# Performance work log

Hardware: AMD Instinct MI355X
Metric: run time of the kernel (lower is better)

## Reference

```python
import jax, jax.numpy as jnp
import numpy as np

EMBED_DIM = 1024
NUM_HEADS = 16
HEAD_DIM = EMBED_DIM // NUM_HEADS  # used only for the softmax scale


def setup_inputs() -> dict:
    key = jax.random.key(0)
    k_x, k_wqkv, k_bqkv, k_wo, k_bo = jax.random.split(key, 5)
    bound_qkv = 1.0 / np.sqrt(EMBED_DIM)
    return {
        "x": jax.random.normal(k_x, (4, 2048, EMBED_DIM), dtype=jnp.float32),
        "W_qkv": jax.random.uniform(k_wqkv, (EMBED_DIM, 3 * EMBED_DIM), jnp.float32, -bound_qkv, bound_qkv),
        "b_qkv": jax.random.uniform(k_bqkv, (3 * EMBED_DIM,), jnp.float32, -bound_qkv, bound_qkv),
        "W_out": jax.random.uniform(k_wo, (EMBED_DIM, EMBED_DIM), jnp.float32, -bound_qkv, bound_qkv),
        "b_out": jax.random.uniform(k_bo, (EMBED_DIM,), jnp.float32, -bound_qkv, bound_qkv),
    }


def reference(x, W_qkv, b_qkv, W_out, b_out):
    # fused QKV projection: [B,S,3E]
    qkv = jnp.einsum("bse,ef->bsf", x, W_qkv) + b_qkv
    q, k, v = jnp.split(qkv, 3, axis=-1)  # each [B,S,E]
    scale = 1.0 / jnp.sqrt(jnp.float32(HEAD_DIM))
    # NOTE: no head reshape — attention over full embed_dim, scale uses head_dim
    scores = jnp.einsum("bqe,bke->bqk", q, k) * scale  # [B,S,S]
    attn = jax.nn.softmax(scores, axis=-1)
    context = jnp.einsum("bqk,bke->bqe", attn, v)  # [B,S,E]
    return jnp.einsum("bse,ef->bsf", context, W_out) + b_out
```

## Files before the change

kernel.cpp:

```cpp
#include <hip/hip_runtime.h>

typedef unsigned short u16;
typedef __bf16   bf16x8 __attribute__((ext_vector_type(8)));
typedef float    f32x4  __attribute__((ext_vector_type(4)));
typedef unsigned short u16x4 __attribute__((ext_vector_type(4)));

__device__ inline float bf2f(u16 u) { return __uint_as_float(((unsigned int)u) << 16); }
__device__ inline u16 f2bf(float f) {
    unsigned int u = __float_as_uint(f);
    u += 0x7FFF + ((u >> 16) & 1);
    return (u16)(u >> 16);
}

__device__ inline void gl2lds16(const u16* g, u16* l) {
    __builtin_amdgcn_global_load_lds(
        (const __attribute__((address_space(1))) void*)g,
        (__attribute__((address_space(3))) void*)l, 16, 0, 0);
}

__global__ void sniff_dtype(const u16* __restrict__ x, int* __restrict__ flag) {
    const int lane = threadIdx.x;
    const unsigned idx = lane * 131072u + 65536u;
    const u16 u = x[idx];
    const int e = (u >> 7) & 0xFF;
    const unsigned long long b = __ballot(e >= 100 && e <= 140);
    if (lane == 0) flag[0] = (__popcll(b) >= 48) ? 0 : 1;
}

__global__ __launch_bounds__(256)
void convx(const void* __restrict__ in, u16* __restrict__ out, const int* __restrict__ flagp) {
    const long i = ((long)blockIdx.x * 256 + threadIdx.x) * 4;
    if (*flagp) {
        f32x4 v = *(const f32x4*)((const float*)in + i);
        u16x4 o; o[0] = f2bf(v[0]); o[1] = f2bf(v[1]); o[2] = f2bf(v[2]); o[3] = f2bf(v[3]);
        *(u16x4*)(out + i) = o;
    } else {
        *(u16x4*)(out + i) = *(const u16x4*)((const u16*)in + i);
    }
}

__global__ __launch_bounds__(256)
void conv_biases(const void* __restrict__ b1, const void* __restrict__ b2,
                 u16* __restrict__ o1, u16* __restrict__ o2,
                 const int* __restrict__ flagp) {
    const int i = blockIdx.x * 256 + threadIdx.x;
    const int f = *flagp;
    if (i < 3072) o1[i] = f ? f2bf(((const float*)b1)[i]) : ((const u16*)b1)[i];
    else { const int j = i - 3072;
           o2[j] = f ? f2bf(((const float*)b2)[j]) : ((const u16*)b2)[j]; }
}

template <int GM, int GN, int WM, int WN, int OUT_MODE, bool HAS_BIAS>
__global__ __launch_bounds__(256, 4)
void gemm_t(const u16* __restrict__ A, const u16* __restrict__ Bt,
            void* __restrict__ Cv, const u16* __restrict__ bias,
            int K, long lda, long ldb, long ldc,
            long aBatch, long bBatch, long cBatch, float scale,
            const int* __restrict__ flagp)
{
    constexpr int BM = GM * WM * 16;
    constexpr int BN = GN * WN * 16;
    constexpr int IA = BM / 32;
    constexpr int IB = BN / 32;
    __shared__ __align__(16) u16 As[BM * 64];
    __shared__ __align__(16) u16 Bs[BN * 64];

    const int outF32 = (OUT_MODE == 2) ? *flagp : OUT_MODE;

    const int tid  = threadIdx.x;
    const int lane = tid & 63;
    const int wave = tid >> 6;
    const long m0 = (long)blockIdx.y * BM;
    const long n0 = (long)blockIdx.x * BN;
    const long bz = blockIdx.z;

    const int sr  = tid >> 3;
    const int qg0 = (tid & 7) ^ (sr & 7);
    const u16* pa[IA];
    const u16* pb[IB];
    u16* la[IA];
    u16* lb[IB];
#pragma unroll
    for (int i = 0; i < IA; ++i) {
        pa[i] = A + bz * aBatch + (m0 + i * 32 + sr) * lda + qg0 * 8;
        la[i] = As + (i * 256 + wave * 64) * 8;
    }
#pragma unroll
    for (int i = 0; i < IB; ++i) {
        pb[i] = Bt + bz * bBatch + (n0 + i * 32 + sr) * ldb + qg0 * 8;
        lb[i] = Bs + (i * 256 + wave * 64) * 8;
    }

    const int wm = (wave / GN) * (WM * 16);
    const int wn = (wave % GN) * (WN * 16);
    const int lr = lane & 15;
    const int hk = lane >> 4;

    int aoff[WM][2], boff[WN][2];
#pragma unroll
    for (int i = 0; i < WM; ++i) {
        const int row = wm + i * 16 + lr, r7 = row & 7;
        aoff[i][0] = row * 64 + ((hk     ^ r7) * 8);
        aoff[i][1] = row * 64 + (((4+hk) ^ r7) * 8);
    }
#pragma unroll
    for (int j = 0; j < WN; ++j) {
        const int row = wn + j * 16 + lr, r7 = row & 7;
        boff[j][0] = row * 64 + ((hk     ^ r7) * 8);
        boff[j][1] = row * 64 + (((4+hk) ^ r7) * 8);
    }

    f32x4 acc[WM][WN] = {};

    for (int kt = 0; kt < K; kt += 64) {
#pragma unroll
        for (int i = 0; i < IA; ++i) { gl2lds16(pa[i], la[i]); pa[i] += 64; }
#pragma unroll
        for (int i = 0; i < IB; ++i) { gl2lds16(pb[i], lb[i]); pb[i] += 64; }
        __syncthreads();

#pragma unroll
        for (int ks = 0; ks < 2; ++ks) {
            bf16x8 af[WM], bf[WN];
#pragma unroll
            for (int i = 0; i < WM; ++i) af[i] = *(const bf16x8*)&As[aoff[i][ks]];
#pragma unroll
            for (int j = 0; j < WN; ++j) bf[j] = *(const bf16x8*)&Bs[boff[j][ks]];
#pragma unroll
            for (int i = 0; i < WM; ++i)
#pragma unroll
                for (int j = 0; j < WN; ++j)
                    acc[i][j] = __builtin_amdgcn_mfma_f32_16x16x32_bf16(af[i], bf[j], acc[i][j], 0, 0, 0);
        }
        __syncthreads();
    }

#pragma unroll
    for (int j = 0; j < WN; ++j) {
        const long c = n0 + wn + j*16 + lr;
        const float bj = HAS_BIAS ? bf2f(bias[c]) : 0.0f;
#pragma unroll
        for (int i = 0; i < WM; ++i) {
            const long rbase = m0 + wm + i*16 + hk * 4;
#pragma unroll
            for (int r = 0; r < 4; ++r) {
                const float v = acc[i][j][r] * scale + bj;
                const long ci = bz * cBatch + (rbase + r) * ldc + c;
                if (outF32) ((float*)Cv)[ci] = v;
                else        ((u16*)Cv)[ci]   = f2bf(v);
            }
        }
    }
}

__global__ __launch_bounds__(256)
void transpose_any(const void* __restrict__ in, u16* __restrict__ out,
                   long inStride, long outStride, const int* __restrict__ flagp)
{
    __shared__ u16 t[32][36];
    const int isF32 = *flagp;
    const int tid = threadIdx.x;
    const long r0 = (long)blockIdx.y * 32;
    const long c0 = (long)blockIdx.x * 32;
    const int r  = tid >> 3;
    const int c4 = (tid & 7) * 4;
    const long base = (r0 + r) * inStride + c0 + c4;
    u16x4 v;
    if (isF32) {
        f32x4 f = *(const f32x4*)((const float*)in + base);
        v[0] = f2bf(f[0]); v[1] = f2bf(f[1]); v[2] = f2bf(f[2]); v[3] = f2bf(f[3]);
    } else {
        v = *(const u16x4*)((const u16*)in + base);
    }
    t[r][c4 + 0] = v[0]; t[r][c4 + 1] = v[1]; t[r][c4 + 2] = v[2]; t[r][c4 + 3] = v[3];
    __syncthreads();
    u16x4 o;
    o[0] = t[c4 + 0][r]; o[1] = t[c4 + 1][r]; o[2] = t[c4 + 2][r]; o[3] = t[c4 + 3][r];
    *(u16x4*)&out[(c0 + r) * outStride + r0 + c4] = o;
}

__global__ __launch_bounds__(256)
void transpose_bf16(const u16* __restrict__ in, u16* __restrict__ out,
                    long inStride, long outStride, long inBatch, long outBatch)
{
    __shared__ u16 t[32][36];
    const int tid = threadIdx.x;
    const long r0 = (long)blockIdx.y * 32;
    const long c0 = (long)blockIdx.x * 32;
    in  += (long)blockIdx.z * inBatch;
    out += (long)blockIdx.z * outBatch;
    const int r  = tid >> 3;
    const int c4 = (tid & 7) * 4;
    u16x4 v = *(const u16x4*)&in[(r0 + r) * inStride + c0 + c4];
    t[r][c4 + 0] = v[0]; t[r][c4 + 1] = v[1]; t[r][c4 + 2] = v[2]; t[r][c4 + 3] = v[3];
    __syncthreads();
    u16x4 o;
    o[0] = t[c4 + 0][r]; o[1] = t[c4 + 1][r]; o[2] = t[c4 + 2][r]; o[3] = t[c4 + 3][r];
    *(u16x4*)&out[(c0 + r) * outStride + r0 + c4] = o;
}

__global__ __launch_bounds__(256)
void softmax_inplace(float* __restrict__ scores)
{
    float* p = scores + (size_t)blockIdx.x * 2048;
    const int tid = threadIdx.x;
    const int wave = tid >> 6, lane = tid & 63;
    float x[8];
#pragma unroll
    for (int i = 0; i < 8; ++i) x[i] = p[tid + i * 256];
    float m = x[0];
#pragma unroll
    for (int i = 1; i < 8; ++i) m = fmaxf(m, x[i]);
#pragma unroll
    for (int o = 32; o; o >>= 1) m = fmaxf(m, __shfl_xor(m, o));
    __shared__ float red[4];
    if (lane == 0) red[wave] = m;
    __syncthreads();
    m = fmaxf(fmaxf(red[0], red[1]), fmaxf(red[2], red[3]));
    float e[8], s = 0.0f;
#pragma unroll
    for (int i = 0; i < 8; ++i) { e[i] = __expf(x[i] - m); s += e[i]; }
#pragma unroll
    for (int o = 32; o; o >>= 1) s += __shfl_xor(s, o);
    __syncthreads();
    if (lane == 0) red[wave] = s;
    __syncthreads();
    s = red[0] + red[1] + red[2] + red[3];
    const float inv = 1.0f / s;
    u16* ob = (u16*)p;
#pragma unroll
    for (int i = 0; i < 8; ++i) ob[tid + i * 256] = f2bf(e[i] * inv);
}

extern "C" void kernel_launch(void* const* d_in, const int* in_sizes, int n_in,
                              void* d_out, int out_size, void* d_ws, size_t ws_size,
                              hipStream_t stream)
{
    const void* x    = d_in[0];
    const void* Wqkv = d_in[1];
    const void* bqkv = d_in[2];
    const void* Wout = d_in[3];
    const void* bout = d_in[4];
    char* ws = (char*)d_ws;

    float* SC    = (float*)(ws);
    u16*   SCu   = (u16*)(ws);
    u16*   xbf   = (u16*)(ws);
    u16*   WqkvT = (u16*)(ws + 16777216);
    u16*   QKV   = (u16*)(ws + 67108864);
    u16*   VT    = (u16*)(ws + 117440512);
    u16*   WoutT = (u16*)(ws + 134217728);
    u16*   bqkvc = (u16*)(ws + 136314880);
    u16*   boutc = (u16*)(ws + 136321024);
    int*   flag  = (int*)(ws + 136323072);

    dim3 blk(256);

    sniff_dtype<<<1, 64, 0, stream>>>((const u16*)x, flag);
    convx<<<8192, blk, 0, stream>>>(x, xbf, flag);
    conv_biases<<<16, blk, 0, stream>>>(bqkv, bout, bqkvc, boutc, flag);
    transpose_any<<<dim3(96, 32), blk, 0, stream>>>(Wqkv, WqkvT, 3072L, 1024L, flag);
    transpose_any<<<dim3(32, 32), blk, 0, stream>>>(Wout, WoutT, 1024L, 1024L, flag);

    gemm_t<2, 2, 4, 4, 0, true><<<dim3(24, 64, 1), blk, 0, stream>>>(
        xbf, WqkvT, QKV, bqkvc, 1024, 1024L, 1024L, 3072L, 0L, 0L, 0L, 1.0f, nullptr);

    transpose_bf16<<<dim3(32, 64, 4), blk, 0, stream>>>(
        QKV + 2048, VT, 3072L, 2048L, 2048L * 3072L, 1024L * 2048L);

    gemm_t<2, 2, 4, 4, 1, false><<<dim3(16, 16, 4), blk, 0, stream>>>(
        QKV, QKV + 1024, SC, nullptr, 1024, 3072L, 3072L, 2048L,
        2048L * 3072L, 2048L * 3072L, 2048L * 2048L, 0.125f, nullptr);

    softmax_inplace<<<dim3(8192), blk, 0, stream>>>(SC);

    gemm_t<4, 1, 2, 4, 0, false><<<dim3(16, 16, 4), blk, 0, stream>>>(
        SCu, VT, SCu + 2048, nullptr, 2048, 4096L, 2048L, 4096L,
        2048L * 4096L, 1024L * 2048L, 2048L * 4096L, 1.0f, nullptr);

    gemm_t<4, 1, 2, 4, 2, true><<<dim3(16, 64, 1), blk, 0, stream>>>(
        SCu + 2048, WoutT, d_out, boutc, 1024, 4096L, 1024L, 1024L,
        0L, 0L, 0L, 1.0f, flag);
}
```

Measured before the change: 298.6 us.

## Fuse softmax into QK^T and PV GEMM epilogues with atomic row sums

Removes the standalone softmax kernel. The QK^T GEMM epilogue now applies exp to the scaled scores, writes bf16 probabilities directly, and accumulates per-row sums with atomicAdd into a zeroed buffer. The PV GEMM epilogue divides by those sums. This avoids writing and re-reading a full fp32 score matrix. The catch is that the max subtraction is dropped, so exp can overflow if scores get large, and the atomics add some contention.

```diff
diff --git a/kernel.cpp b/kernel.cpp
--- a/kernel.cpp
+++ b/kernel.cpp
@@ -25,6 +25,11 @@
     const int e = (u >> 7) & 0xFF;
     const unsigned long long b = __ballot(e >= 100 && e <= 140);
     if (lane == 0) flag[0] = (__popcll(b) >= 48) ? 0 : 1;
+}
+
+__global__ __launch_bounds__(256)
+void zero_f32(float* __restrict__ p) {
+    p[blockIdx.x * 256 + threadIdx.x] = 0.0f;
 }
 
 __global__ __launch_bounds__(256)
@@ -50,13 +55,13 @@
            o2[j] = f ? f2bf(((const float*)b2)[j]) : ((const u16*)b2)[j]; }
 }
 
-template <int GM, int GN, int WM, int WN, int OUT_MODE, bool HAS_BIAS>
+template <int GM, int GN, int WM, int WN, int EPI, int OUT_MODE, bool HAS_BIAS>
 __global__ __launch_bounds__(256, 4)
 void gemm_t(const u16* __restrict__ A, const u16* __restrict__ Bt,
             void* __restrict__ Cv, const u16* __restrict__ bias,
             int K, long lda, long ldb, long ldc,
             long aBatch, long bBatch, long cBatch, float scale,
-            const int* __restrict__ flagp)
+            const int* __restrict__ flagp, float* __restrict__ sums)
 {
     constexpr int BM = GM * WM * 16;
     constexpr int BN = GN * WN * 16;
@@ -135,19 +140,49 @@
         __syncthreads();
     }
 
-#pragma unroll
-    for (int j = 0; j < WN; ++j) {
-        const long c = n0 + wn + j*16 + lr;
-        const float bj = HAS_BIAS ? bf2f(bias[c]) : 0.0f;
+    if (EPI == 1) {
 #pragma unroll
         for (int i = 0; i < WM; ++i) {
-            const long rbase = m0 + wm + i*16 + hk * 4;
 #pragma unroll
             for (int r = 0; r < 4; ++r) {
-                const float v = acc[i][j][r] * scale + bj;
-                const long ci = bz * cBatch + (rbase + r) * ldc + c;
-                if (outF32) ((float*)Cv)[ci] = v;
-                else        ((u16*)Cv)[ci]   = f2bf(v);
+                const long row = m0 + wm + i*16 + hk*4 + r;
+                float s = 0.0f;
+#pragma unroll
+                for (int j = 0; j < WN; ++j) {
+                    const long c = n0 + wn + j*16 + lr;
+                    const float e = __expf(acc[i][j][r] * scale);
+                    ((u16*)Cv)[bz * cBatch + row * ldc + c] = f2bf(e);
+                    s += e;
+                }
+                s += __shfl_xor(s, 1); s += __shfl_xor(s, 2);
+                s += __shfl_xor(s, 4); s += __shfl_xor(s, 8);
+                if (lr == 0) atomicAdd(&sums[bz * 2048 + row], s);
+            }
+        }
+    } else {
+        float inv[WM][4];
+        if (EPI == 2) {
+#pragma unroll
+            for (int i = 0; i < WM; ++i)
+#pragma unroll
+                for (int r = 0; r < 4; ++r)
+                    inv[i][r] = 1.0f / sums[bz * 2048 + m0 + wm + i*16 + hk*4 + r];
+        }
+#pragma unroll
+        for (int j = 0; j < WN; ++j) {
+            const long c = n0 + wn + j*16 + lr;
+            const float bj = HAS_BIAS ? bf2f(bias[c]) : 0.0f;
+#pragma unroll
+            for (int i = 0; i < WM; ++i) {
+                const long rbase = m0 + wm + i*16 + hk * 4;
+#pragma unroll
+                for (int r = 0; r < 4; ++r) {
+                    float v = (EPI == 2) ? acc[i][j][r] * inv[i][r]
+                                         : acc[i][j][r] * scale + bj;
+                    const long ci = bz * cBatch + (rbase + r) * ldc + c;
+                    if (outF32) ((float*)Cv)[ci] = v;
+                    else        ((u16*)Cv)[ci]   = f2bf(v);
+                }
             }
         }
     }
@@ -199,39 +234,6 @@
     *(u16x4*)&out[(c0 + r) * outStride + r0 + c4] = o;
 }
 
-__global__ __launch_bounds__(256)
-void softmax_inplace(float* __restrict__ scores)
-{
-    float* p = scores + (size_t)blockIdx.x * 2048;
-    const int tid = threadIdx.x;
-    const int wave = tid >> 6, lane = tid & 63;
-    float x[8];
-#pragma unroll
-    for (int i = 0; i < 8; ++i) x[i] = p[tid + i * 256];
-    float m = x[0];
-#pragma unroll
-    for (int i = 1; i < 8; ++i) m = fmaxf(m, x[i]);
-#pragma unroll
-    for (int o = 32; o; o >>= 1) m = fmaxf(m, __shfl_xor(m, o));
-    __shared__ float red[4];
-    if (lane == 0) red[wave] = m;
-    __syncthreads();
-    m = fmaxf(fmaxf(red[0], red[1]), fmaxf(red[2], red[3]));
-    float e[8], s = 0.0f;
-#pragma unroll
-    for (int i = 0; i < 8; ++i) { e[i] = __expf(x[i] - m); s += e[i]; }
-#pragma unroll
-    for (int o = 32; o; o >>= 1) s += __shfl_xor(s, o);
-    __syncthreads();
-    if (lane == 0) red[wave] = s;
-    __syncthreads();
-    s = red[0] + red[1] + red[2] + red[3];
-    const float inv = 1.0f / s;
-    u16* ob = (u16*)p;
-#pragma unroll
-    for (int i = 0; i < 8; ++i) ob[tid + i * 256] = f2bf(e[i] * inv);
-}
-
 extern "C" void kernel_launch(void* const* d_in, const int* in_sizes, int n_in,
                               void* d_out, int out_size, void* d_ws, size_t ws_size,
                               hipStream_t stream)
@@ -243,42 +245,43 @@
     const void* bout = d_in[4];
     char* ws = (char*)d_ws;
 
-    float* SC    = (float*)(ws);
-    u16*   SCu   = (u16*)(ws);
     u16*   xbf   = (u16*)(ws);
     u16*   WqkvT = (u16*)(ws + 16777216);
-    u16*   QKV   = (u16*)(ws + 67108864);
-    u16*   VT    = (u16*)(ws + 117440512);
-    u16*   WoutT = (u16*)(ws + 134217728);
-    u16*   bqkvc = (u16*)(ws + 136314880);
-    u16*   boutc = (u16*)(ws + 136321024);
-    int*   flag  = (int*)(ws + 136323072);
+    u16*   P     = (u16*)(ws);
+    u16*   QKV   = (u16*)(ws + 33554432);
+    u16*   VT    = (u16*)(ws + 83886080);
+    u16*   CTX   = (u16*)(ws + 100663296);
+    u16*   WoutT = (u16*)(ws + 117440512);
+    u16*   bqkvc = (u16*)(ws + 119537664);
+    u16*   boutc = (u16*)(ws + 119543808);
+    int*   flag  = (int*)(ws + 119545856);
+    float* sums  = (float*)(ws + 119549952);
 
     dim3 blk(256);
 
     sniff_dtype<<<1, 64, 0, stream>>>((const u16*)x, flag);
+    zero_f32<<<32, blk, 0, stream>>>(sums);
     convx<<<8192, blk, 0, stream>>>(x, xbf, flag);
     conv_biases<<<16, blk, 0, stream>>>(bqkv, bout, bqkvc, boutc, flag);
     transpose_any<<<dim3(96, 32), blk, 0, stream>>>(Wqkv, WqkvT, 3072L, 1024L, flag);
     transpose_any<<<dim3(32, 32), blk, 0, stream>>>(Wout, WoutT, 1024L, 1024L, flag);
 
-    gemm_t<2, 2, 4, 4, 0, true><<<dim3(24, 64, 1), blk, 0, stream>>>(
-        xbf, WqkvT, QKV, bqkvc, 1024, 1024L, 1024L, 3072L, 0L, 0L, 0L, 1.0f, nullptr);
+    gemm_t<2, 2, 4, 4, 0, 0, true><<<dim3(24, 64, 1), blk, 0, stream>>>(
+        xbf, WqkvT, QKV, bqkvc, 1024, 1024L, 1024L, 3072L,
+        0L, 0L, 0L, 1.0f, nullptr, nullptr);
 
     transpose_bf16<<<dim3(32, 64, 4), blk, 0, stream>>>(
         QKV + 2048, VT, 3072L, 2048L, 2048L * 3072L, 1024L * 2048L);
 
-    gemm_t<2, 2, 4, 4, 1, false><<<dim3(16, 16, 4), blk, 0, stream>>>(
-        QKV, QKV + 1024, SC, nullptr, 1024, 3072L, 3072L, 2048L,
-        2048L * 3072L, 2048L * 3072L, 2048L * 2048L, 0.125f, nullptr);
-
-    softmax_inplace<<<dim3(8192), blk, 0, stream>>>(SC);
-
-    gemm_t<4, 1, 2, 4, 0, false><<<dim3(16, 16, 4), blk, 0, stream>>>(
-        SCu, VT, SCu + 2048, nullptr, 2048, 4096L, 2048L, 4096L,
-        2048L * 4096L, 1024L * 2048L, 2048L * 4096L, 1.0f, nullptr);
-
-    gemm_t<4, 1, 2, 4, 2, true><<<dim3(16, 64, 1), blk, 0, stream>>>(
-        SCu + 2048, WoutT, d_out, boutc, 1024, 4096L, 1024L, 1024L,
-        0L, 0L, 0L, 1.0f, flag);
-}
+    gemm_t<2, 2, 4, 4, 1, 0, false><<<dim3(16, 16, 4), blk, 0, stream>>>(
+        QKV, QKV + 1024, P, nullptr, 1024, 3072L, 3072L, 2048L,
+        2048L * 3072L, 2048L * 3072L, 2048L * 2048L, 0.125f, nullptr, sums);
+
+    gemm_t<4, 1, 2, 4, 2, 0, false><<<dim3(16, 16, 4), blk, 0, stream>>>(
+        P, VT, CTX, nullptr, 2048, 2048L, 2048L, 1024L,
+        2048L * 2048L, 1024L * 2048L, 2048L * 1024L, 1.0f, nullptr, sums);
+
+    gemm_t<4, 1, 2, 4, 0, 2, true><<<dim3(16, 64, 1), blk, 0, stream>>>(
+        CTX, WoutT, d_out, boutc, 1024, 1024L, 1024L, 1024L,
+        0L, 0L, 0L, 1.0f, flag, nullptr);
+}
```

Measured after the change: 295.5 us. Within noise of the previous version (-1.0%).
